# Optimization experiments

Measured on AMD Instinct MI355X. Metric: run time of the kernel, lower is better.

The kernel has to match this reference:

```python
import jax, jax.numpy as jnp
import numpy as np

N, E, NMASK, NC = 50000, 600000, 10000, 16
DIMS = [128, 96, 64]
EPS = 1e-5


def _sage(x, src, dst, ew, deg_pos, Wp, bp, Ws, Wn, b):
    # DGL SAGEConv 'pool': m_e = relu(fc_pool(h_src)) * w_e ; neigh = max_e->v m_e
    p = jax.nn.relu(x @ Wp.T + bp)              # [N, din]
    m = p[src] * ew[:, None]                    # [E, din]
    neigh = jax.ops.segment_max(m, dst, num_segments=N)
    neigh = jnp.where(deg_pos, neigh, 0.0)      # zero in-degree -> 0 (DGL convention)
    return jax.nn.relu(x @ Ws.T + neigh @ Wn.T + b)


def setup_inputs() -> dict:
    key = jax.random.key(0)
    ks = iter(jax.random.split(key, 64))
    inp = {}
    inp["x"] = jax.random.normal(next(ks), (N, DIMS[0]), jnp.float32)
    inp["src"] = jax.random.randint(next(ks), (E,), 0, N)
    inp["dst"] = jax.random.randint(next(ks), (E,), 0, N)
    inp["ew"] = jax.random.uniform(next(ks), (E,), jnp.float32)
    inp["mask_nodes"] = jax.random.permutation(next(ks), N)[:NMASK]
    inp["mask_token"] = jax.random.normal(next(ks), (1, DIMS[0]), jnp.float32) * 0.02

    def lin(k, o, i):
        return jax.random.normal(k, (o, i), jnp.float32) * (1.0 / np.sqrt(i))

    enc_pairs = list(zip(DIMS[:-1], DIMS[1:]))              # (128,96),(96,64)
    dec_pairs = [(o, i) for (i, o) in reversed(enc_pairs)]  # (64,96),(96,128)
    for name, pairs in (("enc", enc_pairs), ("dec", dec_pairs)):
        for l, (di, do) in enumerate(pairs):
            inp[f"{name}{l}_Wp"] = lin(next(ks), di, di)
            inp[f"{name}{l}_bp"] = jnp.zeros((di,), jnp.float32)
            inp[f"{name}{l}_Ws"] = lin(next(ks), do, di)
            inp[f"{name}{l}_Wn"] = lin(next(ks), do, di)
            inp[f"{name}{l}_b"] = jnp.zeros((do,), jnp.float32)
    H = DIMS[-1]
    inp["W_e2d"] = lin(next(ks), H, H)
    inp["Wnp"] = lin(next(ks), NC, H)
    inp["bnp"] = jnp.zeros((NC,), jnp.float32)
    inp["ln_g"] = jnp.ones((NC,), jnp.float32)
    inp["ln_b"] = jnp.zeros((NC,), jnp.float32)
    return inp


def reference(x, src, dst, ew, mask_nodes, mask_token,
              enc0_Wp, enc0_bp, enc0_Ws, enc0_Wn, enc0_b,
              enc1_Wp, enc1_bp, enc1_Ws, enc1_Wn, enc1_b,
              dec0_Wp, dec0_bp, dec0_Ws, dec0_Wn, dec0_b,
              dec1_Wp, dec1_bp, dec1_Ws, dec1_Wn, dec1_b,
              W_e2d, Wnp, bnp, ln_g, ln_b):
    deg = jax.ops.segment_sum(jnp.ones((E,), jnp.float32), dst, num_segments=N)
    deg_pos = (deg > 0)[:, None]
    # mask: out_x[mask]=0 then += enc_mask_token  ==  set to token row
    h = x.at[mask_nodes].set(mask_token[0])
    h = _sage(h, src, dst, ew, deg_pos, enc0_Wp, enc0_bp, enc0_Ws, enc0_Wn, enc0_b)
    h = _sage(h, src, dst, ew, deg_pos, enc1_Wp, enc1_bp, enc1_Ws, enc1_Wn, enc1_b)
    # dropout(p=0) is identity
    z = h @ Wnp.T + bnp                              # node_pred linear
    mu = jnp.mean(z, -1, keepdims=True)
    var = jnp.var(z, -1, keepdims=True)
    n_scores = (z - mu) * jax.lax.rsqrt(var + EPS) * ln_g + ln_b
    r = h @ W_e2d.T                                  # encoder_to_decoder (no bias)
    r = _sage(r, src, dst, ew, deg_pos, dec0_Wp, dec0_bp, dec0_Ws, dec0_Wn, dec0_b)
    r = _sage(r, src, dst, ew, deg_pos, dec1_Wp, dec1_bp, dec1_Ws, dec1_Wn, dec1_b)
    return (r[mask_nodes], x[mask_nodes], n_scores)
```

## Files before the change

kernel.cpp:

```cpp
#include <hip/hip_runtime.h>

#define EPS_LN 1e-5f

typedef __attribute__((ext_vector_type(4))) float f32x4;
typedef __attribute__((ext_vector_type(4))) int i32x4;

__device__ inline unsigned short f2bf_rne(float x) {
  unsigned int u = __float_as_uint(x);
  unsigned int r = u + 0x7fffu + ((u >> 16) & 1u);
  return (unsigned short)(r >> 16);
}

__device__ inline float4 bf4_to_f4(uint2 u) {
  float4 f;
  f.x = __uint_as_float(u.x << 16);
  f.y = __uint_as_float(u.x & 0xffff0000u);
  f.z = __uint_as_float(u.y << 16);
  f.w = __uint_as_float(u.y & 0xffff0000u);
  return f;
}

__device__ inline uint2 f4_to_bf4(float4 v) {
  uint2 o;
  o.x = (unsigned)f2bf_rne(v.x) | ((unsigned)f2bf_rne(v.y) << 16);
  o.y = (unsigned)f2bf_rne(v.z) | ((unsigned)f2bf_rne(v.w) << 16);
  return o;
}

__global__ __launch_bounds__(256) void copy_bf16_kernel(const float4* __restrict__ in,
                                                        uint2* __restrict__ out, int n4) {
  int i = blockIdx.x * 256 + threadIdx.x;
  if (i < n4) out[i] = f4_to_bf4(in[i]);
}

__global__ __launch_bounds__(256) void mask_scatter_kernel(const int* __restrict__ mn,
                                                           const float* __restrict__ token,
                                                           unsigned short* __restrict__ H,
                                                           int nmask) {
  int gid = blockIdx.x * 256 + threadIdx.x;
  if (gid >= nmask * 32) return;
  int i = gid >> 5;
  int c4 = (gid & 31) << 2;
  int r = mn[i];
  float4 t = *(const float4*)(token + c4);
  *(uint2*)(H + (size_t)r * 128 + c4) = f4_to_bf4(t);
}

__global__ __launch_bounds__(256) void hist_kernel(const int* __restrict__ dst,
                                                   int* __restrict__ deg, int nE) {
  int e = blockIdx.x * 256 + threadIdx.x;
  if (e < nE) atomicAdd(deg + dst[e], 1);
}

#define SCAN_CHUNK 1024

__global__ __launch_bounds__(256) void blocksum_kernel(const int* __restrict__ deg,
                                                       int* __restrict__ bsum, int n) {
  __shared__ int red[256];
  int base = blockIdx.x * SCAN_CHUNK;
  int tid = threadIdx.x;
  int s = 0;
#pragma unroll
  for (int t = 0; t < SCAN_CHUNK / 256; ++t) {
    int g = base + tid + t * 256;
    if (g < n) s += deg[g];
  }
  red[tid] = s;
  __syncthreads();
  for (int ofs = 128; ofs > 0; ofs >>= 1) {
    if (tid < ofs) red[tid] += red[tid + ofs];
    __syncthreads();
  }
  if (tid == 0) bsum[blockIdx.x] = red[0];
}

__global__ __launch_bounds__(64) void bscan_kernel(const int* __restrict__ bsum,
                                                   int* __restrict__ bbase,
                                                   int* __restrict__ off_n, int nb) {
  int tid = threadIdx.x;
  int v = (tid < nb) ? bsum[tid] : 0;
  int incl = v;
#pragma unroll
  for (int ofs = 1; ofs < 64; ofs <<= 1) {
    int u = __shfl_up(incl, ofs, 64);
    if (tid >= ofs) incl += u;
  }
  if (tid < nb) bbase[tid] = incl - v;
  if (tid == nb - 1) off_n[0] = incl;
}

__global__ __launch_bounds__(256) void chunkscan_kernel(const int* __restrict__ deg,
                                                        const int* __restrict__ bbase,
                                                        int* __restrict__ off, int n) {
  __shared__ int part[256];
  int tid = threadIdx.x;
  int base = blockIdx.x * SCAN_CHUNK;
  int g0 = base + tid * 4;
  int loc[4];
  int s = 0;
#pragma unroll
  for (int j = 0; j < 4; ++j) {
    int g = g0 + j;
    int d = (g < n) ? deg[g] : 0;
    loc[j] = s;
    s += d;
  }
  part[tid] = s;
  __syncthreads();
  for (int ofs = 1; ofs < 256; ofs <<= 1) {
    int v = 0;
    if (tid >= ofs) v = part[tid - ofs];
    __syncthreads();
    if (tid >= ofs) part[tid] += v;
    __syncthreads();
  }
  int pre = (tid == 0) ? 0 : part[tid - 1];
  int b = bbase[blockIdx.x] + pre;
#pragma unroll
  for (int j = 0; j < 4; ++j) {
    int g = g0 + j;
    if (g < n) off[g] = b + loc[j];
  }
}

__global__ __launch_bounds__(256) void perm_scatter_kernel(
    const int* __restrict__ dst, const int* __restrict__ off,
    int* __restrict__ cur, int* __restrict__ perm, int nE) {
  int e = blockIdx.x * 256 + threadIdx.x;
  if (e >= nE) return;
  int d = dst[e];
  int pos = off[d] + atomicAdd(cur + d, 1);
  perm[pos] = e;
}

__global__ __launch_bounds__(256) void esw_build_kernel(
    const int* __restrict__ perm, const int* __restrict__ src,
    const float* __restrict__ ew, int2* __restrict__ esw, int nE) {
  int i = blockIdx.x * 256 + threadIdx.x;
  if (i >= nE) return;
  int e = perm[i];
  esw[i] = make_int2(src[e], __float_as_int(ew[e]));
}

__global__ __launch_bounds__(256) void neigh_csr_kernel(
    const unsigned short* __restrict__ P, const int* __restrict__ off,
    const int2* __restrict__ esw,
    unsigned short* __restrict__ neigh, int din, int lanes, int nN) {
  int gid = blockIdx.x * 256 + threadIdx.x;
  int v = gid / lanes;
  int c = (gid - v * lanes) << 3;
  if (v >= nN) return;
  int jlo = off[v], jhi = off[v + 1];
  float m[8];
#pragma unroll
  for (int t = 0; t < 8; ++t) m[t] = 0.f;
  float n1[8], n2[8], n3[8];
#pragma unroll
  for (int t = 0; t < 8; ++t) { n1[t] = 0.f; n2[t] = 0.f; n3[t] = 0.f; }
  int j = jlo;
  for (; j + 4 <= jhi; j += 4) {
    int2 e0 = esw[j], e1 = esw[j + 1], e2 = esw[j + 2], e3 = esw[j + 3];
    uint4 q0 = *(const uint4*)(P + (size_t)e0.x * din + c);
    uint4 q1 = *(const uint4*)(P + (size_t)e1.x * din + c);
    uint4 q2 = *(const uint4*)(P + (size_t)e2.x * din + c);
    uint4 q3 = *(const uint4*)(P + (size_t)e3.x * din + c);
    float w0 = __int_as_float(e0.y), w1 = __int_as_float(e1.y);
    float w2 = __int_as_float(e2.y), w3 = __int_as_float(e3.y);
    float4 a0 = bf4_to_f4(make_uint2(q0.x, q0.y)), b0 = bf4_to_f4(make_uint2(q0.z, q0.w));
    float4 a1 = bf4_to_f4(make_uint2(q1.x, q1.y)), b1 = bf4_to_f4(make_uint2(q1.z, q1.w));
    float4 a2 = bf4_to_f4(make_uint2(q2.x, q2.y)), b2 = bf4_to_f4(make_uint2(q2.z, q2.w));
    float4 a3 = bf4_to_f4(make_uint2(q3.x, q3.y)), b3 = bf4_to_f4(make_uint2(q3.z, q3.w));
    m[0] = fmaxf(m[0], a0.x * w0); m[1] = fmaxf(m[1], a0.y * w0);
    m[2] = fmaxf(m[2], a0.z * w0); m[3] = fmaxf(m[3], a0.w * w0);
    m[4] = fmaxf(m[4], b0.x * w0); m[5] = fmaxf(m[5], b0.y * w0);
    m[6] = fmaxf(m[6], b0.z * w0); m[7] = fmaxf(m[7], b0.w * w0);
    n1[0] = fmaxf(n1[0], a1.x * w1); n1[1] = fmaxf(n1[1], a1.y * w1);
    n1[2] = fmaxf(n1[2], a1.z * w1); n1[3] = fmaxf(n1[3], a1.w * w1);
    n1[4] = fmaxf(n1[4], b1.x * w1); n1[5] = fmaxf(n1[5], b1.y * w1);
    n1[6] = fmaxf(n1[6], b1.z * w1); n1[7] = fmaxf(n1[7], b1.w * w1);
    n2[0] = fmaxf(n2[0], a2.x * w2); n2[1] = fmaxf(n2[1], a2.y * w2);
    n2[2] = fmaxf(n2[2], a2.z * w2); n2[3] = fmaxf(n2[3], a2.w * w2);
    n2[4] = fmaxf(n2[4], b2.x * w2); n2[5] = fmaxf(n2[5], b2.y * w2);
    n2[6] = fmaxf(n2[6], b2.z * w2); n2[7] = fmaxf(n2[7], b2.w * w2);
    n3[0] = fmaxf(n3[0], a3.x * w3); n3[1] = fmaxf(n3[1], a3.y * w3);
    n3[2] = fmaxf(n3[2], a3.z * w3); n3[3] = fmaxf(n3[3], a3.w * w3);
    n3[4] = fmaxf(n3[4], b3.x * w3); n3[5] = fmaxf(n3[5], b3.y * w3);
    n3[6] = fmaxf(n3[6], b3.z * w3); n3[7] = fmaxf(n3[7], b3.w * w3);
  }
  for (; j < jhi; ++j) {
    int2 e = esw[j];
    float w = __int_as_float(e.y);
    uint4 q = *(const uint4*)(P + (size_t)e.x * din + c);
    float4 a = bf4_to_f4(make_uint2(q.x, q.y)), b = bf4_to_f4(make_uint2(q.z, q.w));
    m[0] = fmaxf(m[0], a.x * w); m[1] = fmaxf(m[1], a.y * w);
    m[2] = fmaxf(m[2], a.z * w); m[3] = fmaxf(m[3], a.w * w);
    m[4] = fmaxf(m[4], b.x * w); m[5] = fmaxf(m[5], b.y * w);
    m[6] = fmaxf(m[6], b.z * w); m[7] = fmaxf(m[7], b.w * w);
  }
#pragma unroll
  for (int t = 0; t < 8; ++t) m[t] = fmaxf(fmaxf(m[t], n1[t]), fmaxf(n2[t], n3[t]));
  uint2 o0 = f4_to_bf4(make_float4(m[0], m[1], m[2], m[3]));
  uint2 o1 = f4_to_bf4(make_float4(m[4], m[5], m[6], m[7]));
  *(uint4*)(neigh + (size_t)v * din + c) = make_uint4(o0.x, o0.y, o1.x, o1.y);
}

__global__ __launch_bounds__(256) void matmul_small_kernel(const float* __restrict__ A,
                                                           const float* __restrict__ B,
                                                           float* __restrict__ C,
                                                           int M, int K, int N) {
  int idx = blockIdx.x * 256 + threadIdx.x;
  if (idx >= M * N) return;
  int o = idx / N, i = idx - o * N;
  float s = 0.f;
  for (int k = 0; k < K; ++k) s += A[o * K + k] * B[k * N + i];
  C[idx] = s;
}

__device__ inline void mfma_b16(f32x4& acc, i32x4 a, i32x4 b) {
  asm volatile("v_mfma_f32_16x16x32_bf16 %0, %1, %2, %0"
               : "+v"(acc)
               : "v"(a), "v"(b));
}

__device__ inline void split_bf16(float x, unsigned short& hi, unsigned short& lo) {
  unsigned int bits = __float_as_uint(x);
  hi = (unsigned short)(bits >> 16);
  float hif = __uint_as_float((unsigned int)hi << 16);
  float res = x - hif;
  lo = (unsigned short)(__float_as_uint(res) >> 16);
}

struct SplitWArgs {
  const float* src[12];
  unsigned short* dh[12];
  unsigned short* dl[12];
  int n[12];
};

__global__ __launch_bounds__(256) void split_w_kernel(SplitWArgs a) {
  int m = blockIdx.y;
  int i = (blockIdx.x * 256 + threadIdx.x) * 4;
  if (i >= a.n[m]) return;
  float4 v = *(const float4*)(a.src[m] + i);
  unsigned short h[4], l[4];
  split_bf16(v.x, h[0], l[0]);
  split_bf16(v.y, h[1], l[1]);
  split_bf16(v.z, h[2], l[2]);
  split_bf16(v.w, h[3], l[3]);
  *(uint2*)(a.dh[m] + i) = make_uint2((unsigned)h[0] | ((unsigned)h[1] << 16),
                                      (unsigned)h[2] | ((unsigned)h[3] << 16));
  *(uint2*)(a.dl[m] + i) = make_uint2((unsigned)l[0] | ((unsigned)l[1] << 16),
                                      (unsigned)l[2] | ((unsigned)l[3] << 16));
}

template <int TNT>
__global__ __launch_bounds__(256) void mfma_gemm_kernel(
    const unsigned short* __restrict__ A1, const unsigned short* __restrict__ Wh1,
    const unsigned short* __restrict__ Wl1, int k1,
    const unsigned short* __restrict__ A2, const unsigned short* __restrict__ Wh2,
    const unsigned short* __restrict__ Wl2, int k2,
    const float* __restrict__ bias, int relu,
    unsigned short* __restrict__ C, int nrows) {
  constexpr int BN = TNT * 16;
  constexpr int WS = 136;
  __shared__ __align__(16) unsigned short Wh[BN][WS];
  __shared__ __align__(16) unsigned short Wl[BN][WS];

  const int tid = threadIdx.x;
  const int lane = tid & 63;
  const int wv = tid >> 6;
  const int lr = lane & 15;
  const int lg = lane >> 4;
  const int row0 = blockIdx.x * 64;
  const int gra = row0 + wv * 16 + lr;

  f32x4 acc[TNT];
#pragma unroll
  for (int t = 0; t < TNT; ++t) acc[t] = (f32x4)(0.f);

  for (int pass = 0; pass < 2; ++pass) {
    const unsigned short* A = pass ? A2 : A1;
    if (A == nullptr) continue;
    const unsigned short* Whp = pass ? Wh2 : Wh1;
    const unsigned short* Wlp = pass ? Wl2 : Wl1;
    const int K = pass ? k2 : k1;

    if (pass) __syncthreads();
    {
      int tot8 = BN * K / 8;
      for (int i = tid; i < tot8; i += 256) {
        int e0 = i * 8;
        int col = e0 / K;
        int kk = e0 - col * K;
        *(uint4*)&Wh[col][kk] = *(const uint4*)(Whp + e0);
        *(uint4*)&Wl[col][kk] = *(const uint4*)(Wlp + e0);
      }
    }
    __syncthreads();

    for (int cb = 0; cb < K; cb += 32) {
      i32x4 a_h = (i32x4)(0);
      if (gra < nrows) a_h = *(const i32x4*)(A + (size_t)gra * K + cb + lg * 8);
#pragma unroll
      for (int t = 0; t < TNT; ++t) {
        i32x4 b_h = *(const i32x4*)&Wh[t * 16 + lr][cb + lg * 8];
        i32x4 b_l = *(const i32x4*)&Wl[t * 16 + lr][cb + lg * 8];
        mfma_b16(acc[t], a_h, b_h);
        mfma_b16(acc[t], a_h, b_l);
      }
    }
  }

  asm volatile("s_nop 7\n\ts_nop 7" ::);

#pragma unroll
  for (int t = 0; t < TNT; ++t) {
    int c = t * 16 + lr;
    float bv = bias ? bias[c] : 0.f;
#pragma unroll
    for (int q = 0; q < 4; ++q) {
      int r = row0 + wv * 16 + lg * 4 + q;
      if (r < nrows) {
        float v = acc[t][q] + bv;
        if (relu) v = fmaxf(v, 0.f);
        C[(size_t)r * BN + c] = f2bf_rne(v);
      }
    }
  }
}

__global__ __launch_bounds__(256) void nodepred_ln_kernel(
    const unsigned short* __restrict__ H, const float* __restrict__ Wnp,
    const float* __restrict__ bnp, const float* __restrict__ g,
    const float* __restrict__ lb, float* __restrict__ out, int nrows) {
  __shared__ float hs[16][64];
  int tid = threadIdx.x;
  int row0 = blockIdx.x * 16;
  {
    int r = tid >> 4;
    int c4 = (tid & 15) << 2;
    int gr = row0 + r;
    float4 v = make_float4(0.f, 0.f, 0.f, 0.f);
    if (gr < nrows) v = bf4_to_f4(*(const uint2*)(H + (size_t)gr * 64 + c4));
    *(float4*)&hs[r][c4] = v;
  }
  __syncthreads();
  int r = tid >> 4, j = tid & 15;
  float z = bnp[j];
  const float* wrow = Wnp + j * 64;
#pragma unroll 8
  for (int k = 0; k < 64; ++k) z += hs[r][k] * wrow[k];
  float s = z, s2 = z * z;
#pragma unroll
  for (int m = 1; m < 16; m <<= 1) {
    s += __shfl_xor(s, m, 16);
    s2 += __shfl_xor(s2, m, 16);
  }
  float mu = s * (1.f / 16.f);
  float var = s2 * (1.f / 16.f) - mu * mu;
  float o = (z - mu) * rsqrtf(var + EPS_LN) * g[j] + lb[j];
  int gr = row0 + r;
  if (gr < nrows) out[(size_t)gr * 16 + j] = o;
}

__global__ __launch_bounds__(256) void gather_out_kernel(
    const int* __restrict__ mn, const unsigned short* __restrict__ R,
    const float* __restrict__ X,
    float* __restrict__ o1, float* __restrict__ o2, int nmask) {
  int gid = blockIdx.x * 256 + threadIdx.x;
  if (gid >= nmask * 32) return;
  int i = gid >> 5, c4 = (gid & 31) << 2;
  int r = mn[i];
  float4 rv = bf4_to_f4(*(const uint2*)(R + (size_t)r * 128 + c4));
  *(float4*)(o1 + (size_t)i * 128 + c4) = rv;
  *(float4*)(o2 + (size_t)i * 128 + c4) = *(const float4*)(X + (size_t)r * 128 + c4);
}

static void launch_gemm(const unsigned short* A1, const unsigned short* Wh1,
                        const unsigned short* Wl1, int k1,
                        const unsigned short* A2, const unsigned short* Wh2,
                        const unsigned short* Wl2, int k2,
                        const float* bias, int relu,
                        unsigned short* C, int m, int nrows, hipStream_t s) {
  int blocks = (nrows + 63) / 64;
  switch (m) {
    case 128:
      mfma_gemm_kernel<8><<<blocks, 256, 0, s>>>(A1, Wh1, Wl1, k1, A2, Wh2, Wl2, k2,
                                                 bias, relu, C, nrows);
      break;
    case 96:
      mfma_gemm_kernel<6><<<blocks, 256, 0, s>>>(A1, Wh1, Wl1, k1, A2, Wh2, Wl2, k2,
                                                 bias, relu, C, nrows);
      break;
    case 64:
      mfma_gemm_kernel<4><<<blocks, 256, 0, s>>>(A1, Wh1, Wl1, k1, A2, Wh2, Wl2, k2,
                                                 bias, relu, C, nrows);
      break;
  }
}

extern "C" void kernel_launch(void* const* d_in, const int* in_sizes, int n_in,
                              void* d_out, int out_size, void* d_ws, size_t ws_size,
                              hipStream_t stream) {
  const float* x = (const float*)d_in[0];
  const int* src = (const int*)d_in[1];
  const int* dst = (const int*)d_in[2];
  const float* ew = (const float*)d_in[3];
  const int* mn = (const int*)d_in[4];
  const float* token = (const float*)d_in[5];

  const float* W[20];
  for (int i = 0; i < 20; ++i) W[i] = (const float*)d_in[6 + i];
  const float* W_e2d = (const float*)d_in[26];
  const float* Wnp = (const float*)d_in[27];
  const float* bnp = (const float*)d_in[28];
  const float* ln_g = (const float*)d_in[29];
  const float* ln_b = (const float*)d_in[30];

  const int Nn = in_sizes[0] / 128;
  const int E = in_sizes[1];
  const int nmask = in_sizes[4];
  const int nb = (Nn + SCAN_CHUNK - 1) / SCAN_CHUNK;

  unsigned short* bufA = (unsigned short*)d_ws;
  unsigned short* bufB = bufA + (size_t)Nn * 128;
  unsigned short* pool16 = bufB + (size_t)Nn * 128;
  unsigned short* neigh16 = pool16 + (size_t)Nn * 128;
  int* deg = (int*)(neigh16 + (size_t)Nn * 128);
  int* cur = deg + Nn;
  int2* esw = (int2*)(cur + Nn);
  int* off = (int*)(esw + E);
  int* bsum = off + Nn + 1;
  int* bbase = bsum + 64;
  int* perm = bbase + 64;
  float* WpP = (float*)(perm + E);
  float* WsP = WpP + 64 * 64;
  unsigned short* wplanes =
      (unsigned short*)(((uintptr_t)(WsP + 96 * 64) + 15) & ~(uintptr_t)15);

  matmul_small_kernel<<<(64 * 64 + 255) / 256, 256, 0, stream>>>(W[10], W_e2d, WpP, 64, 64, 64);
  matmul_small_kernel<<<(96 * 64 + 255) / 256, 256, 0, stream>>>(W[12], W_e2d, WsP, 96, 64, 64);

  const int msz[12] = {128 * 128, 96 * 128, 96 * 128, 96 * 96, 64 * 96, 64 * 96,
                       64 * 64,  96 * 64,  96 * 64,  96 * 96, 128 * 96, 128 * 96};
  const float* msrc[12] = {W[0], W[2], W[3], W[5], W[7], W[8],
                           WpP,  WsP,  W[13], W[15], W[17], W[18]};
  int mtot = 0;
  int moff[12];
  for (int i = 0; i < 12; ++i) { moff[i] = mtot; mtot += msz[i]; }
  unsigned short* wh_[12];
  unsigned short* wl_[12];
  SplitWArgs sa;
  for (int i = 0; i < 12; ++i) {
    wh_[i] = wplanes + moff[i];
    wl_[i] = wplanes + mtot + moff[i];
    sa.src[i] = msrc[i];
    sa.dh[i] = wh_[i];
    sa.dl[i] = wl_[i];
    sa.n[i] = msz[i];
  }
  {
    dim3 grid((128 * 128 / 4 + 255) / 256, 12);
    split_w_kernel<<<grid, 256, 0, stream>>>(sa);
  }

  hipMemsetAsync(deg, 0, (size_t)Nn * 2 * sizeof(int), stream);
  hist_kernel<<<(E + 255) / 256, 256, 0, stream>>>(dst, deg, E);
  blocksum_kernel<<<nb, 256, 0, stream>>>(deg, bsum, Nn);
  bscan_kernel<<<1, 64, 0, stream>>>(bsum, bbase, off + Nn, nb);
  chunkscan_kernel<<<nb, 256, 0, stream>>>(deg, bbase, off, Nn);
  perm_scatter_kernel<<<(E + 255) / 256, 256, 0, stream>>>(dst, off, cur, perm, E);
  esw_build_kernel<<<(E + 255) / 256, 256, 0, stream>>>(perm, src, ew, esw, E);

  {
    int n4 = Nn * 128 / 4;
    copy_bf16_kernel<<<(n4 + 255) / 256, 256, 0, stream>>>((const float4*)x, (uint2*)bufA, n4);
    mask_scatter_kernel<<<(nmask * 32 + 255) / 256, 256, 0, stream>>>(mn, token, bufA, nmask);
  }

  auto run_sage = [&](int ip, int is, int in_, const float* bp, const float* b,
                      int din, int dout) {
    launch_gemm(bufA, wh_[ip], wl_[ip], din, nullptr, nullptr, nullptr, 0,
                bp, 1, pool16, din, Nn, stream);
    int lanes = din >> 3;
    long long tot = (long long)Nn * lanes;
    int nblocks = (int)((tot + 255) / 256);
    neigh_csr_kernel<<<nblocks, 256, 0, stream>>>(pool16, off, esw, neigh16, din, lanes, Nn);
    launch_gemm(bufA, wh_[is], wl_[is], din, neigh16, wh_[in_], wl_[in_], din,
                b, 1, bufB, dout, Nn, stream);
    unsigned short* t = bufA; bufA = bufB; bufB = t;
  };

  run_sage(0, 1, 2, W[1], W[4], 128, 96);
  run_sage(3, 4, 5, W[6], W[9], 96, 64);

  float* out_r = (float*)d_out;
  float* out_x = out_r + (size_t)nmask * 128;
  float* out_ns = out_x + (size_t)nmask * 128;
  nodepred_ln_kernel<<<(Nn + 15) / 16, 256, 0, stream>>>(bufA, Wnp, bnp, ln_g, ln_b, out_ns, Nn);

  run_sage(6, 7, 8, W[11], W[14], 64, 96);
  run_sage(9, 10, 11, W[16], W[19], 96, 128);

  gather_out_kernel<<<(nmask * 32 + 255) / 256, 256, 0, stream>>>(mn, bufA, x, out_r, out_x, nmask);
}
```

Before: 381.1 us.

## Hold weight fragments in registers and tile GEMM waves as 2x2

The GEMM kernel no longer stages the split-bf16 weights through shared memory with block barriers. Each wave now loads its column-half of the hi/lo weight fragments straight into registers and computes two 16-row tiles, so every A fragment is reused across half the columns and every weight fragment across two row tiles. K becomes a template parameter so the loops fully unroll. The cost is much higher register pressure (for 128x128, 2*4*4 i32x4 weight registers plus accumulators), which may cut occupancy, and every wave loads weights redundantly from global/L2.

```diff
diff --git a/kernel.cpp b/kernel.cpp
--- a/kernel.cpp
+++ b/kernel.cpp
@@ -253,80 +253,85 @@
                                       (unsigned)l[2] | ((unsigned)l[3] << 16));
 }
 
-template <int TNT>
+template <int TNT, int K>
 __global__ __launch_bounds__(256) void mfma_gemm_kernel(
     const unsigned short* __restrict__ A1, const unsigned short* __restrict__ Wh1,
-    const unsigned short* __restrict__ Wl1, int k1,
+    const unsigned short* __restrict__ Wl1,
     const unsigned short* __restrict__ A2, const unsigned short* __restrict__ Wh2,
-    const unsigned short* __restrict__ Wl2, int k2,
+    const unsigned short* __restrict__ Wl2,
     const float* __restrict__ bias, int relu,
     unsigned short* __restrict__ C, int nrows) {
   constexpr int BN = TNT * 16;
-  constexpr int WS = 136;
-  __shared__ __align__(16) unsigned short Wh[BN][WS];
-  __shared__ __align__(16) unsigned short Wl[BN][WS];
+  constexpr int BN2 = BN / 2;
+  constexpr int NC = TNT / 2;
+  constexpr int KC = K / 32;
 
   const int tid = threadIdx.x;
   const int lane = tid & 63;
   const int wv = tid >> 6;
+  const int wr = wv & 1;
+  const int wc = wv >> 1;
   const int lr = lane & 15;
   const int lg = lane >> 4;
   const int row0 = blockIdx.x * 64;
-  const int gra = row0 + wv * 16 + lr;
-
-  f32x4 acc[TNT];
-#pragma unroll
-  for (int t = 0; t < TNT; ++t) acc[t] = (f32x4)(0.f);
+
+  f32x4 acc[2][NC];
+#pragma unroll
+  for (int rf = 0; rf < 2; ++rf)
+#pragma unroll
+    for (int cf = 0; cf < NC; ++cf) acc[rf][cf] = (f32x4)(0.f);
 
   for (int pass = 0; pass < 2; ++pass) {
     const unsigned short* A = pass ? A2 : A1;
     if (A == nullptr) continue;
     const unsigned short* Whp = pass ? Wh2 : Wh1;
     const unsigned short* Wlp = pass ? Wl2 : Wl1;
-    const int K = pass ? k2 : k1;
-
-    if (pass) __syncthreads();
-    {
-      int tot8 = BN * K / 8;
-      for (int i = tid; i < tot8; i += 256) {
-        int e0 = i * 8;
-        int col = e0 / K;
-        int kk = e0 - col * K;
-        *(uint4*)&Wh[col][kk] = *(const uint4*)(Whp + e0);
-        *(uint4*)&Wl[col][kk] = *(const uint4*)(Wlp + e0);
+
+    i32x4 wh[NC][KC], wl[NC][KC];
+#pragma unroll
+    for (int cf = 0; cf < NC; ++cf)
+#pragma unroll
+      for (int kc = 0; kc < KC; ++kc) {
+        size_t o = (size_t)(wc * BN2 + cf * 16 + lr) * K + kc * 32 + lg * 8;
+        wh[cf][kc] = *(const i32x4*)(Whp + o);
+        wl[cf][kc] = *(const i32x4*)(Wlp + o);
+      }
+
+    const int gr0 = row0 + wr * 32 + lr;
+    const int gr1 = gr0 + 16;
+#pragma unroll
+    for (int kc = 0; kc < KC; ++kc) {
+      i32x4 a0 = (i32x4)(0), a1 = (i32x4)(0);
+      if (gr0 < nrows) a0 = *(const i32x4*)(A + (size_t)gr0 * K + kc * 32 + lg * 8);
+      if (gr1 < nrows) a1 = *(const i32x4*)(A + (size_t)gr1 * K + kc * 32 + lg * 8);
+#pragma unroll
+      for (int cf = 0; cf < NC; ++cf) {
+        mfma_b16(acc[0][cf], a0, wh[cf][kc]);
+        mfma_b16(acc[0][cf], a0, wl[cf][kc]);
+        mfma_b16(acc[1][cf], a1, wh[cf][kc]);
+        mfma_b16(acc[1][cf], a1, wl[cf][kc]);
       }
     }
-    __syncthreads();
-
-    for (int cb = 0; cb < K; cb += 32) {
-      i32x4 a_h = (i32x4)(0);
-      if (gra < nrows) a_h = *(const i32x4*)(A + (size_t)gra * K + cb + lg * 8);
-#pragma unroll
-      for (int t = 0; t < TNT; ++t) {
-        i32x4 b_h = *(const i32x4*)&Wh[t * 16 + lr][cb + lg * 8];
-        i32x4 b_l = *(const i32x4*)&Wl[t * 16 + lr][cb + lg * 8];
-        mfma_b16(acc[t], a_h, b_h);
-        mfma_b16(acc[t], a_h, b_l);
+  }
+
+  asm volatile("s_nop 7\n\ts_nop 7" ::);
+
+#pragma unroll
+  for (int rf = 0; rf < 2; ++rf)
+#pragma unroll
+    for (int cf = 0; cf < NC; ++cf) {
+      int c = wc * BN2 + cf * 16 + lr;
+      float bv = bias ? bias[c] : 0.f;
+#pragma unroll
+      for (int q = 0; q < 4; ++q) {
+        int r = row0 + wr * 32 + rf * 16 + lg * 4 + q;
+        if (r < nrows) {
+          float v = acc[rf][cf][q] + bv;
+          if (relu) v = fmaxf(v, 0.f);
+          C[(size_t)r * BN + c] = f2bf_rne(v);
+        }
       }
     }
-  }
-
-  asm volatile("s_nop 7\n\ts_nop 7" ::);
-
-#pragma unroll
-  for (int t = 0; t < TNT; ++t) {
-    int c = t * 16 + lr;
-    float bv = bias ? bias[c] : 0.f;
-#pragma unroll
-    for (int q = 0; q < 4; ++q) {
-      int r = row0 + wv * 16 + lg * 4 + q;
-      if (r < nrows) {
-        float v = acc[t][q] + bv;
-        if (relu) v = fmaxf(v, 0.f);
-        C[(size_t)r * BN + c] = f2bf_rne(v);
-      }
-    }
-  }
 }
 
 __global__ __launch_bounds__(256) void nodepred_ln_kernel(
@@ -377,26 +382,23 @@
 }
 
 static void launch_gemm(const unsigned short* A1, const unsigned short* Wh1,
-                        const unsigned short* Wl1, int k1,
+                        const unsigned short* Wl1,
                         const unsigned short* A2, const unsigned short* Wh2,
-                        const unsigned short* Wl2, int k2,
+                        const unsigned short* Wl2,
                         const float* bias, int relu,
-                        unsigned short* C, int m, int nrows, hipStream_t s) {
+                        unsigned short* C, int m, int K, int nrows, hipStream_t s) {
   int blocks = (nrows + 63) / 64;
-  switch (m) {
-    case 128:
-      mfma_gemm_kernel<8><<<blocks, 256, 0, s>>>(A1, Wh1, Wl1, k1, A2, Wh2, Wl2, k2,
-                                                 bias, relu, C, nrows);
-      break;
-    case 96:
-      mfma_gemm_kernel<6><<<blocks, 256, 0, s>>>(A1, Wh1, Wl1, k1, A2, Wh2, Wl2, k2,
-                                                 bias, relu, C, nrows);
-      break;
-    case 64:
-      mfma_gemm_kernel<4><<<blocks, 256, 0, s>>>(A1, Wh1, Wl1, k1, A2, Wh2, Wl2, k2,
-                                                 bias, relu, C, nrows);
-      break;
-  }
+#define GEMM_CASE(TNT, KK)                                                   \
+  mfma_gemm_kernel<TNT, KK><<<blocks, 256, 0, s>>>(A1, Wh1, Wl1, A2, Wh2,    \
+                                                   Wl2, bias, relu, C, nrows)
+  if (m == 128 && K == 128) GEMM_CASE(8, 128);
+  else if (m == 96 && K == 128) GEMM_CASE(6, 128);
+  else if (m == 96 && K == 96) GEMM_CASE(6, 96);
+  else if (m == 64 && K == 96) GEMM_CASE(4, 96);
+  else if (m == 64 && K == 64) GEMM_CASE(4, 64);
+  else if (m == 96 && K == 64) GEMM_CASE(6, 64);
+  else if (m == 128 && K == 96) GEMM_CASE(8, 96);
+#undef GEMM_CASE
 }
 
 extern "C" void kernel_launch(void* const* d_in, const int* in_sizes, int n_in,
@@ -480,14 +482,14 @@
 
   auto run_sage = [&](int ip, int is, int in_, const float* bp, const float* b,
                       int din, int dout) {
-    launch_gemm(bufA, wh_[ip], wl_[ip], din, nullptr, nullptr, nullptr, 0,
-                bp, 1, pool16, din, Nn, stream);
+    launch_gemm(bufA, wh_[ip], wl_[ip], nullptr, nullptr, nullptr,
+                bp, 1, pool16, din, din, Nn, stream);
     int lanes = din >> 3;
     long long tot = (long long)Nn * lanes;
     int nblocks = (int)((tot + 255) / 256);
     neigh_csr_kernel<<<nblocks, 256, 0, stream>>>(pool16, off, esw, neigh16, din, lanes, Nn);
-    launch_gemm(bufA, wh_[is], wl_[is], din, neigh16, wh_[in_], wl_[in_], din,
-                b, 1, bufB, dout, Nn, stream);
+    launch_gemm(bufA, wh_[is], wl_[is], neigh16, wh_[in_], wl_[in_],
+                b, 1, bufB, dout, din, Nn, stream);
     unsigned short* t = bufA; bufA = bufB; bufB = t;
   };
 
```

After: 405.2 us. 6.3% more time.
